# Optimization experiments

Measured on AMD Instinct MI355X. Metric: run time of the kernel, lower is better.

## Reference

```python
import jax, jax.numpy as jnp
import numpy as np

LN_EPS = 1e-12


def setup_inputs() -> dict:
    key = jax.random.key(0)
    k1, k2, k3, k4 = jax.random.split(key, 4)
    B, H, L, D = 2, 12, 2048, 64
    q = jax.random.normal(k1, (B, H, L, D), dtype=jnp.float32)
    k = jax.random.normal(k2, (B, H, L, D), dtype=jnp.float32)
    v = jax.random.normal(k3, (B, H, L, D), dtype=jnp.float32)
    mask = jax.random.randint(k4, (1, 1, L, L), 0, 2).astype(jnp.int32)
    gamma = jnp.ones((D,), dtype=jnp.float32)
    beta = jnp.zeros((D,), dtype=jnp.float32)
    return {"q": q, "k": k, "v": v, "mask": mask, "gamma": gamma, "beta": beta}


def reference(q, k, v, mask, gamma, beta):
    # score = q @ k^T  -> [B, H, L, L]
    score = jnp.einsum("bhqd,bhkd->bhqk", q, k)
    # masked_fill(mask == 0, -10000)
    score = jnp.where(mask == 0, jnp.float32(-10000.0), score)
    # result = score @ v -> [B, H, L, D]  (no softmax)
    result = jnp.einsum("bhqk,bhkd->bhqd", score, v)
    # layer norm over the last dim (d_tensor)
    mean = jnp.mean(result, axis=-1, keepdims=True)
    var = jnp.var(result, axis=-1, keepdims=True)
    normed = (result - mean) / jnp.sqrt(var + LN_EPS)
    return normed * gamma + beta
```

## Files before the change

### kernel.cpp

```cpp
#include <hip/hip_runtime.h>

#define SEQ 2048
#define HD 64
#define NBH 24
#define ROWB 144

#define MB_OFF   0
#define MB_BYTES (32 * 32 * 512)
#define QB_OFF   (MB_OFF + MB_BYTES)
#define QK_BYTES (NBH * SEQ * HD * 2)
#define KB_OFF   (QB_OFF + QK_BYTES)
#define VT_OFF   (KB_OFF + QK_BYTES)
#define WS_NEED  ((size_t)(VT_OFF + QK_BYTES))

typedef __bf16 bfrag8 __attribute__((ext_vector_type(8)));
typedef __bf16 bf16x4 __attribute__((ext_vector_type(4)));
typedef float  floatx4 __attribute__((ext_vector_type(4)));
typedef float  floatx16 __attribute__((ext_vector_type(16)));

__device__ __forceinline__ floatx4 mfma_16x16x32(bfrag8 a, bfrag8 b, floatx4 c) {
    return __builtin_amdgcn_mfma_f32_16x16x32_bf16(a, b, c, 0, 0, 0);
}
__device__ __forceinline__ floatx16 mfma_32x32x16(bfrag8 a, bfrag8 b, floatx16 c) {
    return __builtin_amdgcn_mfma_f32_32x32x16_bf16(a, b, c, 0, 0, 0);
}

__global__ __launch_bounds__(256)
void prep_kernel(const float* __restrict__ qp, const float* __restrict__ kp,
                 const float* __restrict__ vp, const int* __restrict__ maskp,
                 unsigned char* __restrict__ ws)
{
    __shared__ __attribute__((aligned(16))) unsigned char parena[64 * 68 * 4];
    const int t = threadIdx.x;
    const int b = blockIdx.x;

    if (b < 1536) {
        int gt  = b * 256 + t;
        int row = gt >> 3;
        int c   = gt & 7;
        const floatx4* qs = (const floatx4*)(qp + row * 64 + c * 8);
        const floatx4* ks = (const floatx4*)(kp + row * 64 + c * 8);
        floatx4 q0 = qs[0], q1 = qs[1];
        floatx4 k0 = ks[0], k1 = ks[1];
        bfrag8 qpk, kpk;
        #pragma unroll
        for (int i = 0; i < 4; ++i) {
            qpk[i] = (__bf16)q0[i]; qpk[4 + i] = (__bf16)q1[i];
            kpk[i] = (__bf16)k0[i]; kpk[4 + i] = (__bf16)k1[i];
        }
        *(bfrag8*)(ws + QB_OFF + row * 128 + c * 16) = qpk;
        *(bfrag8*)(ws + KB_OFF + row * 128 + c * 16) = kpk;
    } else if (b < 2304) {
        int bb = b - 1536, bh = bb >> 5, kt = bb & 31;
        float* lf = (float*)parena;
        const floatx4* vg = (const floatx4*)(vp + (bh * SEQ + kt * 64) * 64);
        #pragma unroll
        for (int it = 0; it < 4; ++it) {
            int f = t + it * 256;
            int r = f >> 4, c4 = f & 15;
            floatx4 val = vg[f];
            #pragma unroll
            for (int i = 0; i < 4; ++i) lf[r * 68 + c4 * 4 + i] = val[i];
        }
        __syncthreads();
        int d = t >> 2, kseg = t & 3;
        unsigned char* tb = ws + VT_OFF + (size_t)(bh * 32 + kt) * 8192 + d * 128;
        #pragma unroll
        for (int jj = 0; jj < 2; ++jj) {
            bfrag8 pk;
            #pragma unroll
            for (int e = 0; e < 8; ++e)
                pk[e] = (__bf16)lf[(kseg * 16 + jj * 8 + e) * 68 + d];
            *(bfrag8*)(tb + (kseg * 2 + jj) * 16) = pk;
        }
    } else {
        int cc = b - 2304, qtb = cc >> 5, kt = cc & 31;
        const int w = t >> 6, lane = t & 63;
        #pragma unroll
        for (int it = 0; it < 16; ++it) {
            int rr = it * 4 + w;
            unsigned long long bl = __ballot(maskp[(qtb * 64 + rr) * SEQ + kt * 64 + lane] != 0);
            if (lane == 0)
                *(unsigned long long*)(ws + MB_OFF + (size_t)((qtb * 32 + kt) * 64 + rr) * 8) = bl;
        }
    }
}

__global__ __launch_bounds__(256, 3)
void normattn_main(const unsigned char* __restrict__ ws,
                   const float* __restrict__ gammap, const float* __restrict__ betap,
                   float* __restrict__ outp)
{
    __shared__ __attribute__((aligned(16))) unsigned char sK[2][64 * ROWB];
    __shared__ __attribute__((aligned(16))) unsigned char sV[2][64 * ROWB];

    const int tid  = threadIdx.x;
    const int w    = tid >> 6;
    const int lane = tid & 63;
    const int l32  = lane & 31;
    const int hi   = lane >> 5;
    const int qh   = w & 1;
    const int kh   = w >> 1;
    const int qtb  = blockIdx.x;
    const int bh   = blockIdx.y;
    const int q0   = qtb * 64;

    const unsigned char* gKb = ws + KB_OFF + (size_t)(bh * SEQ) * 128;
    const unsigned char* gVb = ws + VT_OFF + (size_t)(bh * 32) * 8192;
    const unsigned char* gMb = ws + MB_OFF + (size_t)(qtb * 32) * 512;

    bfrag8 qb[4];
    #pragma unroll
    for (int dstep = 0; dstep < 4; ++dstep)
        qb[dstep] = *(const bfrag8*)(ws + QB_OFF +
                        (size_t)(bh * SEQ + q0 + qh * 32 + l32) * 128 + dstep * 32 + hi * 16);

    floatx16 acc[2];
    acc[0] = (floatx16)0.0f;
    acc[1] = (floatx16)0.0f;

    const int sr0 = tid >> 3, sc0 = tid & 7;
    const int sr1 = (tid + 256) >> 3, sc1 = tid & 7;

    auto load_tile = [&](int kt, bfrag8 (&kr)[2], bfrag8 (&vr)[2]) {
        const unsigned char* gK = gKb + (size_t)kt * 8192;
        const unsigned char* gV = gVb + (size_t)kt * 8192;
        kr[0] = *(const bfrag8*)(gK + tid * 16);
        kr[1] = *(const bfrag8*)(gK + (tid + 256) * 16);
        vr[0] = *(const bfrag8*)(gV + tid * 16);
        vr[1] = *(const bfrag8*)(gV + (tid + 256) * 16);
    };
    auto write_tile = [&](int s, bfrag8 (&kr)[2], bfrag8 (&vr)[2]) {
        *(bfrag8*)(&sK[s][0] + sr0 * ROWB + sc0 * 16) = kr[0];
        *(bfrag8*)(&sK[s][0] + sr1 * ROWB + sc1 * 16) = kr[1];
        *(bfrag8*)(&sV[s][0] + sr0 * ROWB + sc0 * 16) = vr[0];
        *(bfrag8*)(&sV[s][0] + sr1 * ROWB + sc1 * 16) = vr[1];
    };

    {
        bfrag8 k0r[2], v0r[2], k1r[2], v1r[2];
        load_tile(0, k0r, v0r);
        load_tile(1, k1r, v1r);
        write_tile(0, k0r, v0r);
        write_tile(1, k1r, v1r);
    }
    asm volatile("s_waitcnt lgkmcnt(0)" ::: "memory");
    asm volatile("s_barrier" ::: "memory");

    const unsigned char* kbase = &sK[0][0] + (kh * 32 + l32) * ROWB + hi * 16;
    const unsigned char* vbase = &sV[0][0] + l32 * ROWB + kh * 64 + hi * 16;

    for (int kt = 0; kt < 32; ++kt) {
        const int slot = kt & 1;
        bfrag8 kN[2], vN[2];
        if (kt < 30) load_tile(kt + 2, kN, vN);

        const unsigned long long mrow =
            *(const unsigned long long*)(gMb + (size_t)kt * 512 + (qh * 32 + l32) * 8);

        floatx16 st = (floatx16)0.0f;
        const unsigned char* cK = kbase + slot * (64 * ROWB);
        #pragma unroll
        for (int dstep = 0; dstep < 4; ++dstep) {
            bfrag8 ka = *(const bfrag8*)(cK + dstep * 32);
            st = mfma_32x32x16(ka, qb[dstep], st);
        }

        const unsigned bits = (unsigned)(mrow >> (kh * 32 + 4 * hi));
        unsigned u[8];
        #pragma unroll
        for (int j = 0; j < 8; ++j) {
            const int kl0 = 2 * (j & 1) + 8 * (j >> 1);
            float a = ((bits >> kl0) & 1u) ? st[2 * j] : -10000.0f;
            float b = ((bits >> (kl0 + 1)) & 1u) ? st[2 * j + 1] : -10000.0f;
            asm("v_cvt_pk_bf16_f32 %0, %1, %2" : "=v"(u[j]) : "v"(a), "v"(b));
        }
        asm("v_permlane32_swap_b32 %0, %1" : "+v"(u[0]), "+v"(u[2]));
        asm("v_permlane32_swap_b32 %0, %1" : "+v"(u[1]), "+v"(u[3]));
        asm("v_permlane32_swap_b32 %0, %1" : "+v"(u[4]), "+v"(u[6]));
        asm("v_permlane32_swap_b32 %0, %1" : "+v"(u[5]), "+v"(u[7]));
        union { unsigned int w4[4]; bfrag8 f; } c0, c1;
        c0.w4[0] = u[0]; c0.w4[1] = u[1]; c0.w4[2] = u[2]; c0.w4[3] = u[3];
        c1.w4[0] = u[4]; c1.w4[1] = u[5]; c1.w4[2] = u[6]; c1.w4[3] = u[7];

        const unsigned char* cV = vbase + slot * (64 * ROWB);
        #pragma unroll
        for (int dh = 0; dh < 2; ++dh) {
            bfrag8 va0 = *(const bfrag8*)(cV + dh * 32 * ROWB);
            bfrag8 va1 = *(const bfrag8*)(cV + dh * 32 * ROWB + 32);
            acc[dh] = mfma_32x32x16(va0, c0.f, acc[dh]);
            acc[dh] = mfma_32x32x16(va1, c1.f, acc[dh]);
        }

        asm volatile("s_waitcnt lgkmcnt(0)" ::: "memory");
        asm volatile("s_barrier" ::: "memory");
        if (kt < 30) write_tile(slot, kN, vN);
    }

    float* ex = (float*)&sK[0][0];
    const int exb = (qh * 64 + lane) * 32;
    if (kh == 1) {
        #pragma unroll
        for (int dh = 0; dh < 2; ++dh)
            #pragma unroll
            for (int jj = 0; jj < 4; ++jj) {
                floatx4 t;
                #pragma unroll
                for (int e = 0; e < 4; ++e) t[e] = acc[dh][jj * 4 + e];
                *(floatx4*)(ex + exb + (((dh * 4 + jj) ^ (lane & 7)) * 4)) = t;
            }
    }
    __syncthreads();
    if (kh == 0) {
        #pragma unroll
        for (int dh = 0; dh < 2; ++dh)
            #pragma unroll
            for (int jj = 0; jj < 4; ++jj) {
                floatx4 t = *(const floatx4*)(ex + exb + (((dh * 4 + jj) ^ (lane & 7)) * 4));
                #pragma unroll
                for (int e = 0; e < 4; ++e) acc[dh][jj * 4 + e] += t[e];
            }
        float s = 0.0f, s2 = 0.0f;
        #pragma unroll
        for (int dh = 0; dh < 2; ++dh)
            #pragma unroll
            for (int r = 0; r < 16; ++r) { float x = acc[dh][r]; s += x; s2 += x * x; }
        s  += __shfl_xor(s, 32);
        s2 += __shfl_xor(s2, 32);
        float mean = s * (1.0f / 64.0f);
        float var  = s2 * (1.0f / 64.0f) - mean * mean;
        float rstd = rsqrtf(var + 1e-12f);
        float* orow = outp + (size_t)(bh * SEQ + q0 + qh * 32 + l32) * 64;
        #pragma unroll
        for (int dh = 0; dh < 2; ++dh)
            #pragma unroll
            for (int jj = 0; jj < 4; ++jj) {
                const int d0 = dh * 32 + jj * 8 + 4 * hi;
                floatx4 gg = *(const floatx4*)(gammap + d0);
                floatx4 bb = *(const floatx4*)(betap + d0);
                floatx4 o;
                #pragma unroll
                for (int e = 0; e < 4; ++e)
                    o[e] = (acc[dh][jj * 4 + e] - mean) * rstd * gg[e] + bb[e];
                *(floatx4*)(orow + d0) = o;
            }
    }
}

#define KROW 72
#define SROW 40
__global__ __launch_bounds__(256, 4)
void normattn_fallback(const float* __restrict__ qp, const float* __restrict__ kp,
                       const float* __restrict__ vp, const int* __restrict__ maskp,
                       const float* __restrict__ gammap, const float* __restrict__ betap,
                       float* __restrict__ outp)
{
    __shared__ __attribute__((aligned(16))) __bf16 sQ[64 * KROW];
    __shared__ __attribute__((aligned(16))) __bf16 sK[64 * KROW];
    __shared__ __attribute__((aligned(16))) __bf16 sV[64 * KROW];
    __shared__ __attribute__((aligned(16))) __bf16 sS[4][16 * SROW];
    __shared__ __attribute__((aligned(8)))  unsigned int sMw[64][2];

    const int tid = threadIdx.x, wave = tid >> 6, lane = tid & 63;
    const int quad = lane >> 4, l16 = lane & 15;
    const int q0 = blockIdx.x * 64, bh = blockIdx.y;
    const int base = bh * SEQ * HD;
    {
        const floatx4* qg = (const floatx4*)(qp + base + q0 * HD);
        #pragma unroll
        for (int it = 0; it < 4; ++it) {
            int idx = tid + it * 256, r = idx >> 4, c = idx & 15;
            floatx4 val = qg[idx];
            bf16x4 pk = {(__bf16)val[0], (__bf16)val[1], (__bf16)val[2], (__bf16)val[3]};
            *(bf16x4*)&sQ[r * KROW + c * 4] = pk;
        }
    }
    __syncthreads();
    bfrag8 qa0 = *(const bfrag8*)&sQ[(wave * 16 + l16) * KROW + quad * 8];
    bfrag8 qa1 = *(const bfrag8*)&sQ[(wave * 16 + l16) * KROW + quad * 8 + 32];
    floatx4 acc[4];
    #pragma unroll
    for (int i = 0; i < 4; ++i) acc[i] = (floatx4)0.0f;
    const int qrow_loc = wave * 16 + quad * 4;
    const int qrb = q0 + qrow_loc;
    for (int kb = 0; kb < SEQ; kb += 64) {
        __syncthreads();
        {
            const floatx4* kg = (const floatx4*)(kp + base + kb * HD);
            #pragma unroll
            for (int it = 0; it < 4; ++it) {
                int idx = tid + it * 256, r = idx >> 4, c = idx & 15;
                floatx4 val = kg[idx];
                bf16x4 pk = {(__bf16)val[0], (__bf16)val[1], (__bf16)val[2], (__bf16)val[3]};
                *(bf16x4*)&sK[r * KROW + c * 4] = pk;
            }
        }
        {
            int d = tid & 63;
            #pragma unroll
            for (int it = 0; it < 4; ++it) {
                int k4 = (tid >> 6) + it * 4;
                bf16x4 pk;
                #pragma unroll
                for (int i = 0; i < 4; ++i) pk[i] = (__bf16)vp[base + (kb + k4 * 4 + i) * HD + d];
                *(bf16x4*)&sV[d * KROW + k4 * 4] = pk;
            }
        }
        #pragma unroll
        for (int it = 0; it < 16; ++it) {
            int rr = it * 4 + wave;
            unsigned long long bl = __ballot(maskp[(q0 + rr) * SEQ + kb + lane] != 0);
            if (lane == 0) { sMw[rr][0] = (unsigned)bl; sMw[rr][1] = (unsigned)(bl >> 32); }
        }
        __syncthreads();
        unsigned long long mrow[4];
        #pragma unroll
        for (int r = 0; r < 4; ++r) mrow[r] = *(const unsigned long long*)&sMw[qrow_loc + r][0];
        #pragma unroll
        for (int kc = 0; kc < 64; kc += 32) {
            floatx4 s0 = (floatx4)0.0f, s1 = (floatx4)0.0f;
            bfrag8 b00 = *(const bfrag8*)&sK[(kc + l16) * KROW + quad * 8];
            bfrag8 b01 = *(const bfrag8*)&sK[(kc + l16) * KROW + quad * 8 + 32];
            bfrag8 b10 = *(const bfrag8*)&sK[(kc + 16 + l16) * KROW + quad * 8];
            bfrag8 b11 = *(const bfrag8*)&sK[(kc + 16 + l16) * KROW + quad * 8 + 32];
            s0 = mfma_16x16x32(qa0, b00, s0);
            s0 = mfma_16x16x32(qa1, b01, s0);
            s1 = mfma_16x16x32(qa0, b10, s1);
            s1 = mfma_16x16x32(qa1, b11, s1);
            #pragma unroll
            for (int r = 0; r < 4; ++r) {
                float v0 = ((mrow[r] >> (kc + l16)) & 1ull) ? s0[r] : -10000.0f;
                float v1 = ((mrow[r] >> (kc + 16 + l16)) & 1ull) ? s1[r] : -10000.0f;
                sS[wave][(quad * 4 + r) * SROW + l16] = (__bf16)v0;
                sS[wave][(quad * 4 + r) * SROW + 16 + l16] = (__bf16)v1;
            }
            asm volatile("s_waitcnt lgkmcnt(0)" ::: "memory");
            bfrag8 pa = *(const bfrag8*)&sS[wave][l16 * SROW + quad * 8];
            #pragma unroll
            for (int nt = 0; nt < 4; ++nt) {
                bfrag8 vb = *(const bfrag8*)&sV[(nt * 16 + l16) * KROW + kc + quad * 8];
                acc[nt] = mfma_16x16x32(pa, vb, acc[nt]);
            }
        }
    }
    float g[4], bt[4];
    #pragma unroll
    for (int nt = 0; nt < 4; ++nt) { g[nt] = gammap[nt * 16 + l16]; bt[nt] = betap[nt * 16 + l16]; }
    #pragma unroll
    for (int r = 0; r < 4; ++r) {
        float s = 0.0f, s2 = 0.0f;
        #pragma unroll
        for (int nt = 0; nt < 4; ++nt) { float xx = acc[nt][r]; s += xx; s2 += xx * xx; }
        #pragma unroll
        for (int off = 1; off < 16; off <<= 1) { s += __shfl_xor(s, off); s2 += __shfl_xor(s2, off); }
        float mean = s * (1.0f / 64.0f);
        float var = s2 * (1.0f / 64.0f) - mean * mean;
        float rstd = rsqrtf(var + 1e-12f);
        float* orow = outp + base + (qrb + r) * HD;
        #pragma unroll
        for (int nt = 0; nt < 4; ++nt)
            orow[nt * 16 + l16] = (acc[nt][r] - mean) * rstd * g[nt] + bt[nt];
    }
}

extern "C" void kernel_launch(void* const* d_in, const int* in_sizes, int n_in,
                              void* d_out, int out_size, void* d_ws, size_t ws_size,
                              hipStream_t stream) {
    const float* q     = (const float*)d_in[0];
    const float* k     = (const float*)d_in[1];
    const float* v     = (const float*)d_in[2];
    const int*   mask  = (const int*)d_in[3];
    const float* gamma = (const float*)d_in[4];
    const float* beta  = (const float*)d_in[5];
    float* out = (float*)d_out;

    dim3 grid(32, NBH);
    if (ws_size >= WS_NEED) {
        unsigned char* ws = (unsigned char*)d_ws;
        prep_kernel<<<3328, 256, 0, stream>>>(q, k, v, mask, ws);
        normattn_main<<<grid, 256, 0, stream>>>(ws, gamma, beta, out);
    } else {
        normattn_fallback<<<grid, 256, 0, stream>>>(q, k, v, mask, gamma, beta, out);
    }
}
```

Measured before the change: 141.7 us.

## Load K/V MFMA fragments directly from global memory, dropping LDS staging

```diff
diff --git a/kernel.cpp b/kernel.cpp
--- a/kernel.cpp
+++ b/kernel.cpp
@@ -3,7 +3,6 @@
 #define SEQ 2048
 #define HD 64
 #define NBH 24
-#define ROWB 144
 
 #define MB_OFF   0
 #define MB_BYTES (32 * 32 * 512)
@@ -91,8 +90,7 @@
                    const float* __restrict__ gammap, const float* __restrict__ betap,
                    float* __restrict__ outp)
 {
-    __shared__ __attribute__((aligned(16))) unsigned char sK[2][64 * ROWB];
-    __shared__ __attribute__((aligned(16))) unsigned char sV[2][64 * ROWB];
+    __shared__ __attribute__((aligned(16))) float ex[4096];
 
     const int tid  = threadIdx.x;
     const int w    = tid >> 6;
@@ -105,9 +103,12 @@
     const int bh   = blockIdx.y;
     const int q0   = qtb * 64;
 
-    const unsigned char* gKb = ws + KB_OFF + (size_t)(bh * SEQ) * 128;
-    const unsigned char* gVb = ws + VT_OFF + (size_t)(bh * 32) * 8192;
-    const unsigned char* gMb = ws + MB_OFF + (size_t)(qtb * 32) * 512;
+    const unsigned char* gK = ws + KB_OFF +
+        ((size_t)(bh * SEQ) + kh * 32 + l32) * 128 + hi * 16;
+    const unsigned char* gV = ws + VT_OFF + (size_t)(bh * 32) * 8192 +
+        l32 * 128 + kh * 64 + hi * 16;
+    const unsigned char* gM = ws + MB_OFF + (size_t)(qtb * 32) * 512 +
+        (qh * 32 + l32) * 8;
 
     bfrag8 qb[4];
     #pragma unroll
@@ -119,54 +120,24 @@
     acc[0] = (floatx16)0.0f;
     acc[1] = (floatx16)0.0f;
 
-    const int sr0 = tid >> 3, sc0 = tid & 7;
-    const int sr1 = (tid + 256) >> 3, sc1 = tid & 7;
-
-    auto load_tile = [&](int kt, bfrag8 (&kr)[2], bfrag8 (&vr)[2]) {
-        const unsigned char* gK = gKb + (size_t)kt * 8192;
-        const unsigned char* gV = gVb + (size_t)kt * 8192;
-        kr[0] = *(const bfrag8*)(gK + tid * 16);
-        kr[1] = *(const bfrag8*)(gK + (tid + 256) * 16);
-        vr[0] = *(const bfrag8*)(gV + tid * 16);
-        vr[1] = *(const bfrag8*)(gV + (tid + 256) * 16);
+    auto load_frags = [&](int kt, bfrag8 (&ka)[4], bfrag8 (&va)[4], unsigned long long& mr) {
+        const unsigned char* pk = gK + (size_t)kt * 8192;
+        const unsigned char* pv = gV + (size_t)kt * 8192;
+        #pragma unroll
+        for (int d = 0; d < 4; ++d) ka[d] = *(const bfrag8*)(pk + d * 32);
+        #pragma unroll
+        for (int j = 0; j < 4; ++j)
+            va[j] = *(const bfrag8*)(pv + (j >> 1) * 4096 + (j & 1) * 32);
+        mr = *(const unsigned long long*)(gM + (size_t)kt * 512);
     };
-    auto write_tile = [&](int s, bfrag8 (&kr)[2], bfrag8 (&vr)[2]) {
-        *(bfrag8*)(&sK[s][0] + sr0 * ROWB + sc0 * 16) = kr[0];
-        *(bfrag8*)(&sK[s][0] + sr1 * ROWB + sc1 * 16) = kr[1];
-        *(bfrag8*)(&sV[s][0] + sr0 * ROWB + sc0 * 16) = vr[0];
-        *(bfrag8*)(&sV[s][0] + sr1 * ROWB + sc1 * 16) = vr[1];
-    };
-
-    {
-        bfrag8 k0r[2], v0r[2], k1r[2], v1r[2];
-        load_tile(0, k0r, v0r);
-        load_tile(1, k1r, v1r);
-        write_tile(0, k0r, v0r);
-        write_tile(1, k1r, v1r);
-    }
-    asm volatile("s_waitcnt lgkmcnt(0)" ::: "memory");
-    asm volatile("s_barrier" ::: "memory");
-
-    const unsigned char* kbase = &sK[0][0] + (kh * 32 + l32) * ROWB + hi * 16;
-    const unsigned char* vbase = &sV[0][0] + l32 * ROWB + kh * 64 + hi * 16;
-
-    for (int kt = 0; kt < 32; ++kt) {
-        const int slot = kt & 1;
-        bfrag8 kN[2], vN[2];
-        if (kt < 30) load_tile(kt + 2, kN, vN);
-
-        const unsigned long long mrow =
-            *(const unsigned long long*)(gMb + (size_t)kt * 512 + (qh * 32 + l32) * 8);
-
+
+    auto compute = [&](const bfrag8 (&ka)[4], const bfrag8 (&va)[4], unsigned long long mr) {
         floatx16 st = (floatx16)0.0f;
-        const unsigned char* cK = kbase + slot * (64 * ROWB);
-        #pragma unroll
-        for (int dstep = 0; dstep < 4; ++dstep) {
-            bfrag8 ka = *(const bfrag8*)(cK + dstep * 32);
-            st = mfma_32x32x16(ka, qb[dstep], st);
-        }
-
-        const unsigned bits = (unsigned)(mrow >> (kh * 32 + 4 * hi));
+        #pragma unroll
+        for (int dstep = 0; dstep < 4; ++dstep)
+            st = mfma_32x32x16(ka[dstep], qb[dstep], st);
+
+        const unsigned bits = (unsigned)(mr >> (kh * 32 + 4 * hi));
         unsigned u[8];
         #pragma unroll
         for (int j = 0; j < 8; ++j) {
@@ -183,21 +154,23 @@
         c0.w4[0] = u[0]; c0.w4[1] = u[1]; c0.w4[2] = u[2]; c0.w4[3] = u[3];
         c1.w4[0] = u[4]; c1.w4[1] = u[5]; c1.w4[2] = u[6]; c1.w4[3] = u[7];
 
-        const unsigned char* cV = vbase + slot * (64 * ROWB);
-        #pragma unroll
-        for (int dh = 0; dh < 2; ++dh) {
-            bfrag8 va0 = *(const bfrag8*)(cV + dh * 32 * ROWB);
-            bfrag8 va1 = *(const bfrag8*)(cV + dh * 32 * ROWB + 32);
-            acc[dh] = mfma_32x32x16(va0, c0.f, acc[dh]);
-            acc[dh] = mfma_32x32x16(va1, c1.f, acc[dh]);
-        }
-
-        asm volatile("s_waitcnt lgkmcnt(0)" ::: "memory");
-        asm volatile("s_barrier" ::: "memory");
-        if (kt < 30) write_tile(slot, kN, vN);
-    }
-
-    float* ex = (float*)&sK[0][0];
+        acc[0] = mfma_32x32x16(va[0], c0.f, acc[0]);
+        acc[0] = mfma_32x32x16(va[1], c1.f, acc[0]);
+        acc[1] = mfma_32x32x16(va[2], c0.f, acc[1]);
+        acc[1] = mfma_32x32x16(va[3], c1.f, acc[1]);
+    };
+
+    bfrag8 kaA[4], vaA[4], kaB[4], vaB[4];
+    unsigned long long mA, mB;
+    load_frags(0, kaA, vaA, mA);
+    load_frags(1, kaB, vaB, mB);
+    for (int i = 0; i < 16; ++i) {
+        compute(kaA, vaA, mA);
+        if (i < 15) load_frags(2 * i + 2, kaA, vaA, mA);
+        compute(kaB, vaB, mB);
+        if (i < 15) load_frags(2 * i + 3, kaB, vaB, mB);
+    }
+
     const int exb = (qh * 64 + lane) * 32;
     if (kh == 1) {
         #pragma unroll
```

After: 195.4 us. 37.9% more time.
